# Kernel tuning notes

Hardware: AMD Instinct MI355X
Metric: run time of the kernel (lower is better)

Reference implementation:

```python
import jax, jax.numpy as jnp
import numpy as np

B, N, D_IN, D_OUT, D_EDGE = 2, 512, 128, 128, 32
NEG_SLOPE = 0.2  # GATv2 LeakyReLU default


def _glorot(k, shape):
    lim = np.sqrt(6.0 / (shape[0] + shape[1]))
    return jax.random.uniform(k, shape, jnp.float32, -lim, lim)


def setup_inputs() -> dict:
    key = jax.random.key(0)
    ks = jax.random.split(key, 8)
    return {
        "node_features": jax.random.normal(ks[0], (B, N, D_IN), jnp.float32),
        "adj": jax.random.uniform(ks[1], (B, N, N)) < 0.1,  # sparse-ish dense adjacency
        "edge_features": jax.random.normal(ks[2], (B, N, N, D_EDGE), jnp.float32),
        "mask": jnp.ones((B, N), dtype=bool),
        "W_l": _glorot(ks[3], (D_IN, D_OUT)),   # source (lin_l)
        "b_l": jnp.zeros((D_OUT,), jnp.float32),
        "W_r": _glorot(ks[4], (D_IN, D_OUT)),   # target (lin_r)
        "b_r": jnp.zeros((D_OUT,), jnp.float32),
        "W_e": _glorot(ks[5], (D_EDGE, D_OUT)), # lin_edge (no bias)
        "att": _glorot(ks[6], (1, D_OUT))[0],   # attention vector [D_OUT]
        "bias": jnp.zeros((D_OUT,), jnp.float32),
    }


def _gatv2_dense(x, adj, e, mask, W_l, b_l, W_r, b_r, W_e, att, bias):
    # add self-loops (dense GAT convention)
    adj = adj | jnp.eye(N, dtype=bool)
    x_l = x @ W_l + b_l              # [B,N,D] source transform
    x_r = x @ W_r + b_r              # [B,N,D] target transform
    e_t = e @ W_e                    # [B,N,N,D] edge transform
    # edge (j -> i): pre[b,i,j,:] = x_l[b,j] + x_r[b,i] + e_t[b,i,j]
    pre = x_l[:, None, :, :] + x_r[:, :, None, :] + e_t
    score = jnp.einsum('bijd,d->bij', jax.nn.leaky_relu(pre, NEG_SLOPE), att)
    score = jnp.where(adj, score, -jnp.inf)
    alpha = jax.nn.softmax(score, axis=-1)  # softmax over neighbors j
    out = jnp.einsum('bij,bjd->bid', alpha, x_l) + bias
    return jnp.where(mask[:, :, None], out, 0.0)


def reference(node_features, adj, edge_features, mask, W_l, b_l, W_r, b_r, W_e, att, bias):
    return jax.nn.silu(
        _gatv2_dense(node_features, adj, edge_features, mask,
                     W_l, b_l, W_r, b_r, W_e, att, bias)
    )
```

## Files before the change

kernel.cpp:

```cpp
#include <hip/hip_runtime.h>
#include <math.h>

#define BATCH 2
#define NNODE 512
#define DIN   128
#define DOUT  128
#define DE    32
#define NEG   0.2f
#define TI    8
#define TJ    64
#define TIB   8

typedef __attribute__((ext_vector_type(8))) short bf16x8;
typedef __attribute__((ext_vector_type(4))) float f32x4;

__device__ inline short f2bf(float f) {
    union { float f; unsigned u; } v; v.f = f;
    unsigned r = v.u + 0x7fffu + ((v.u >> 16) & 1u);
    return (short)(r >> 16);
}

__global__ __launch_bounds__(256) void xlr_kernel(
    const float* __restrict__ x,  const float* __restrict__ Wl,
    const float* __restrict__ bl, const float* __restrict__ Wr,
    const float* __restrict__ br, float* __restrict__ xl,
    float* __restrict__ xr)
{
    const int r0 = blockIdx.x * 4;
    const int d  = threadIdx.x & 127;
    const int hv = threadIdx.x >> 7;
    __shared__ float xs[4][DIN];
    for (int idx = threadIdx.x; idx < 4 * DIN; idx += 256)
        xs[idx >> 7][idx & 127] = x[(size_t)r0 * DIN + idx];
    __syncthreads();
    const int ra = 2 * hv, rb = ra + 1;
    float al0 = bl[d], al1 = al0, ar0 = br[d], ar1 = ar0;
    #pragma unroll 4
    for (int k = 0; k < DIN; ++k) {
        const float wl = Wl[k * DOUT + d], wr = Wr[k * DOUT + d];
        const float xa = xs[ra][k], xb = xs[rb][k];
        al0 = fmaf(xa, wl, al0); al1 = fmaf(xb, wl, al1);
        ar0 = fmaf(xa, wr, ar0); ar1 = fmaf(xb, wr, ar1);
    }
    xl[(size_t)(r0 + ra) * DOUT + d] = al0;
    xl[(size_t)(r0 + rb) * DOUT + d] = al1;
    xr[(size_t)(r0 + ra) * DOUT + d] = ar0;
    xr[(size_t)(r0 + rb) * DOUT + d] = ar1;
}

__global__ __launch_bounds__(256, 4) void score_kernel(
    const float* __restrict__ xl, const float* __restrict__ xr,
    const void* __restrict__ adjv, const float* __restrict__ e,
    const float* __restrict__ We, const float* __restrict__ att,
    float* __restrict__ sc)
{
    const int bid = blockIdx.x;
    const int jT  = bid & 7;
    const int iT  = (bid >> 3) & 63;
    const int b   = bid >> 9;
    const int i0  = iT * TI, j0 = jT * TJ;
    const int t    = threadIdx.x;
    const int wave = t >> 6;
    const int lane = t & 63;
    const int col  = lane & 15;
    const int g    = lane >> 4;

    __shared__ short WeT_s[DOUT][DE];
    __shared__ float xr_s[TI][DOUT];
    __shared__ float att_s[DOUT];
    __shared__ int   mflag[2];

    if (t < 2) mflag[t] = 0;
    for (int idx = t; idx < DE * DOUT; idx += 256) {
        const int k = idx >> 7, d = idx & 127;
        WeT_s[d][k] = f2bf(We[idx]);
    }
    for (int idx = t; idx < TI * DOUT; idx += 256) {
        const int ii = idx >> 7, d = idx & 127;
        xr_s[ii][d] = xr[(size_t)(b * NNODE + i0 + ii) * DOUT + d];
    }
    if (t < DOUT) att_s[t] = att[t];
    {
        const unsigned* aw = (const unsigned*)adjv;
        unsigned sawF = 0, sawG = 0;
        #pragma unroll
        for (int k = 0; k < 16; ++k) {
            const unsigned w = aw[t + 256 * k];
            sawF |= (w == 0x3f800000u);
            sawG |= (w > 1u);
        }
        if (sawF) atomicOr(&mflag[0], 1);
        if (sawG) atomicOr(&mflag[1], 1);
    }

    float xlv[32];
    {
        const float* xb = xl + (size_t)(b * NNODE + j0 + wave * 16 + g * 4) * DOUT + col;
        #pragma unroll
        for (int dt = 0; dt < 8; ++dt)
            #pragma unroll
            for (int r = 0; r < 4; ++r)
                xlv[dt * 4 + r] = xb[(size_t)r * DOUT + dt * 16];
    }
    __syncthreads();
    const int byteMode = (!mflag[0] && mflag[1]) ? 1 : 0;

    bf16x8 bf[8];
    float  atv[8];
    #pragma unroll
    for (int dt = 0; dt < 8; ++dt) {
        bf[dt]  = *(const bf16x8*)&WeT_s[dt * 16 + col][g * 8];
        atv[dt] = att_s[dt * 16 + col];
    }

    const int jw = j0 + wave * 16;
    const float* ebase = e + ((size_t)(b * NNODE + i0) * NNODE + jw + col) * DE + g * 8;
    const size_t estep = (size_t)NNODE * DE;

    f32x4 a0 = *(const f32x4*)ebase;
    f32x4 a1 = *(const f32x4*)(ebase + 4);

    for (int i = 0; i < TI; ++i) {
        f32x4 a0n, a1n;
        if (i + 1 < TI) {
            const float* apn = ebase + (size_t)(i + 1) * estep;
            a0n = *(const f32x4*)apn;
            a1n = *(const f32x4*)(apn + 4);
        }
        bf16x8 af;
        af[0] = f2bf(a0[0]); af[1] = f2bf(a0[1]);
        af[2] = f2bf(a0[2]); af[3] = f2bf(a0[3]);
        af[4] = f2bf(a1[0]); af[5] = f2bf(a1[1]);
        af[6] = f2bf(a1[2]); af[7] = f2bf(a1[3]);

        const f32x4 z = {0.f, 0.f, 0.f, 0.f};
        float part[4] = {0.f, 0.f, 0.f, 0.f};
        #pragma unroll
        for (int dt = 0; dt < 8; ++dt) {
            const f32x4 c = __builtin_amdgcn_mfma_f32_16x16x32_bf16(af, bf[dt], z, 0, 0, 0);
            const float xrv = xr_s[i][dt * 16 + col];
            #pragma unroll
            for (int r = 0; r < 4; ++r) {
                float p = c[r] + xrv + xlv[dt * 4 + r];
                p = fmaxf(p, NEG * p);
                part[r] = fmaf(atv[dt], p, part[r]);
            }
        }
        #pragma unroll
        for (int r = 0; r < 4; ++r) {
            part[r] += __shfl_xor(part[r], 1, 64);
            part[r] += __shfl_xor(part[r], 2, 64);
            part[r] += __shfl_xor(part[r], 4, 64);
            part[r] += __shfl_xor(part[r], 8, 64);
        }
        if (col == 0) {
            const int ig = i0 + i;
            const int jb = jw + g * 4;
            const unsigned char* aB = (const unsigned char*)adjv + (size_t)(b * NNODE + ig) * NNODE;
            const unsigned*      aW = (const unsigned*)adjv + (size_t)(b * NNODE + ig) * NNODE;
            float4 v;
            float* vp = (float*)&v;
            #pragma unroll
            for (int r = 0; r < 4; ++r) {
                const int j = jb + r;
                const bool conn = (j == ig) ||
                    (byteMode ? (aB[j] != 0) : (aW[j] != 0));
                vp[r] = conn ? part[r] : -1e30f;
            }
            *(float4*)&sc[(size_t)(b * NNODE + ig) * NNODE + jb] = v;
        }
        a0 = a0n; a1 = a1n;
    }
}

__global__ __launch_bounds__(256) void agg_kernel(
    const float* __restrict__ xl, const float* __restrict__ sc,
    const void* __restrict__ adjv, const void* __restrict__ maskv,
    const float* __restrict__ bias, float* __restrict__ out)
{
    const int bid = blockIdx.x;
    const int dh  = bid & 1;
    const int iT  = (bid >> 1) & 63;
    const int b   = bid >> 7;
    const int i0  = iT * TIB, d0 = dh * 64;
    const int t    = threadIdx.x;
    const int wave = t >> 6;
    const int lane = t & 63;

    __shared__ float al_s[TIB][NNODE];
    __shared__ int   mflag[2];

    if (t < 2) mflag[t] = 0;
    {
        const unsigned* aw = (const unsigned*)adjv;
        unsigned sawF = 0, sawG = 0;
        #pragma unroll
        for (int k = 0; k < 16; ++k) {
            const unsigned w = aw[t + 256 * k];
            sawF |= (w == 0x3f800000u);
            sawG |= (w > 1u);
        }
        if (sawF) atomicOr(&mflag[0], 1);
        if (sawG) atomicOr(&mflag[1], 1);
    }
    for (int idx = t; idx < TIB * NNODE; idx += 256) {
        const int r = idx >> 9, jj = idx & 511;
        al_s[r][jj] = sc[(size_t)(b * NNODE + i0 + r) * NNODE + jj];
    }
    __syncthreads();
    const int byteMode = (!mflag[0] && mflag[1]) ? 1 : 0;

    float invs[2];
    #pragma unroll
    for (int q = 0; q < 2; ++q) {
        const int rr = wave + 4 * q;
        float v[8], m = -1e30f;
        #pragma unroll
        for (int k = 0; k < 8; ++k) {
            v[k] = al_s[rr][lane + 64 * k];
            m = fmaxf(m, v[k]);
        }
        #pragma unroll
        for (int off = 32; off; off >>= 1) m = fmaxf(m, __shfl_xor(m, off, 64));
        float s = 0.f;
        #pragma unroll
        for (int k = 0; k < 8; ++k) {
            const float ex = __expf(v[k] - m);
            al_s[rr][lane + 64 * k] = ex;
            s += ex;
        }
        #pragma unroll
        for (int off = 32; off; off >>= 1) s += __shfl_xor(s, off, 64);
        invs[q] = 1.f / s;
    }

    const int d = d0 + lane;
    const float* xb = xl + (size_t)b * NNODE * DOUT + d;
    float a0 = 0.f, a0b = 0.f, a1 = 0.f, a1b = 0.f;
    for (int j = 0; j < NNODE; j += 2) {
        const float x0 = xb[(size_t)j * DOUT];
        const float x1 = xb[(size_t)(j + 1) * DOUT];
        a0  = fmaf(al_s[wave][j],     x0, a0);
        a0b = fmaf(al_s[wave][j + 1], x1, a0b);
        a1  = fmaf(al_s[wave + 4][j],     x0, a1);
        a1b = fmaf(al_s[wave + 4][j + 1], x1, a1b);
    }
    const float bv = bias[d];
    #pragma unroll
    for (int q = 0; q < 2; ++q) {
        const int row = i0 + wave + 4 * q;
        const int mi  = b * NNODE + row;
        const bool mv = byteMode ? (((const unsigned char*)maskv)[mi] != 0)
                                 : (((const unsigned*)maskv)[mi] != 0);
        float val = (q == 0 ? a0 + a0b : a1 + a1b) * invs[q] + bv;
        if (!mv) val = 0.f;
        val = val / (1.f + __expf(-val));
        out[(size_t)mi * DOUT + d] = val;
    }
}

extern "C" void kernel_launch(void* const* d_in, const int* in_sizes, int n_in,
                              void* d_out, int out_size, void* d_ws, size_t ws_size,
                              hipStream_t stream)
{
    const float* x    = (const float*)d_in[0];
    const void*  adj  = d_in[1];
    const float* e    = (const float*)d_in[2];
    const void*  mask = d_in[3];
    const float* Wl   = (const float*)d_in[4];
    const float* bl   = (const float*)d_in[5];
    const float* Wr   = (const float*)d_in[6];
    const float* br   = (const float*)d_in[7];
    const float* We   = (const float*)d_in[8];
    const float* att  = (const float*)d_in[9];
    const float* bias = (const float*)d_in[10];
    float*       out  = (float*)d_out;

    float* xl = (float*)d_ws;
    float* xr = xl + (size_t)BATCH * NNODE * DOUT;
    float* sc = xr + (size_t)BATCH * NNODE * DOUT;

    xlr_kernel<<<(BATCH * NNODE) / 4, 256, 0, stream>>>(x, Wl, bl, Wr, br, xl, xr);
    score_kernel<<<BATCH * (NNODE / TI) * (NNODE / TJ), 256, 0, stream>>>(
        xl, xr, adj, e, We, att, sc);
    agg_kernel<<<BATCH * (NNODE / TIB) * 2, 256, 0, stream>>>(
        xl, sc, adj, mask, bias, out);
}
```

Measured before the change: 58.58 us.

## Fold x_l into MFMA accumulator, use DPP row reductions, halve agg row tile

```diff
diff --git a/kernel.cpp b/kernel.cpp
--- a/kernel.cpp
+++ b/kernel.cpp
@@ -9,7 +9,7 @@
 #define NEG   0.2f
 #define TI    8
 #define TJ    64
-#define TIB   8
+#define TIB   4
 
 typedef __attribute__((ext_vector_type(8))) short bf16x8;
 typedef __attribute__((ext_vector_type(4))) float f32x4;
@@ -18,6 +18,19 @@
     union { float f; unsigned u; } v; v.f = f;
     unsigned r = v.u + 0x7fffu + ((v.u >> 16) & 1u);
     return (short)(r >> 16);
+}
+
+template<int CTRL>
+__device__ inline float dpp_add(float x) {
+    const int y = __builtin_amdgcn_update_dpp(0, __float_as_int(x), CTRL, 0xF, 0xF, false);
+    return x + __int_as_float(y);
+}
+__device__ inline float row16_sum(float x) {
+    x = dpp_add<0x128>(x);
+    x = dpp_add<0x124>(x);
+    x = dpp_add<0x122>(x);
+    x = dpp_add<0x121>(x);
+    return x;
 }
 
 __global__ __launch_bounds__(256) void xlr_kernel(
@@ -93,14 +106,14 @@
         if (sawG) atomicOr(&mflag[1], 1);
     }
 
-    float xlv[32];
+    f32x4 xlv4[8];
     {
         const float* xb = xl + (size_t)(b * NNODE + j0 + wave * 16 + g * 4) * DOUT + col;
         #pragma unroll
         for (int dt = 0; dt < 8; ++dt)
             #pragma unroll
             for (int r = 0; r < 4; ++r)
-                xlv[dt * 4 + r] = xb[(size_t)r * DOUT + dt * 16];
+                xlv4[dt][r] = xb[(size_t)r * DOUT + dt * 16];
     }
     __syncthreads();
     const int byteMode = (!mflag[0] && mflag[1]) ? 1 : 0;
@@ -133,26 +146,22 @@
         af[4] = f2bf(a1[0]); af[5] = f2bf(a1[1]);
         af[6] = f2bf(a1[2]); af[7] = f2bf(a1[3]);
 
-        const f32x4 z = {0.f, 0.f, 0.f, 0.f};
         float part[4] = {0.f, 0.f, 0.f, 0.f};
         #pragma unroll
         for (int dt = 0; dt < 8; ++dt) {
-            const f32x4 c = __builtin_amdgcn_mfma_f32_16x16x32_bf16(af, bf[dt], z, 0, 0, 0);
+            const f32x4 c = __builtin_amdgcn_mfma_f32_16x16x32_bf16(af, bf[dt], xlv4[dt], 0, 0, 0);
             const float xrv = xr_s[i][dt * 16 + col];
             #pragma unroll
             for (int r = 0; r < 4; ++r) {
-                float p = c[r] + xrv + xlv[dt * 4 + r];
+                float p = c[r] + xrv;
                 p = fmaxf(p, NEG * p);
                 part[r] = fmaf(atv[dt], p, part[r]);
             }
         }
         #pragma unroll
-        for (int r = 0; r < 4; ++r) {
-            part[r] += __shfl_xor(part[r], 1, 64);
-            part[r] += __shfl_xor(part[r], 2, 64);
-            part[r] += __shfl_xor(part[r], 4, 64);
-            part[r] += __shfl_xor(part[r], 8, 64);
-        }
+        for (int r = 0; r < 4; ++r)
+            part[r] = row16_sum(part[r]);
+
         if (col == 0) {
             const int ig = i0 + i;
             const int jb = jw + g * 4;
@@ -180,8 +189,8 @@
 {
     const int bid = blockIdx.x;
     const int dh  = bid & 1;
-    const int iT  = (bid >> 1) & 63;
-    const int b   = bid >> 7;
+    const int iT  = (bid >> 1) & 127;
+    const int b   = bid >> 8;
     const int i0  = iT * TIB, d0 = dh * 64;
     const int t    = threadIdx.x;
     const int wave = t >> 6;
@@ -210,14 +219,12 @@
     __syncthreads();
     const int byteMode = (!mflag[0] && mflag[1]) ? 1 : 0;
 
-    float invs[2];
-    #pragma unroll
-    for (int q = 0; q < 2; ++q) {
-        const int rr = wave + 4 * q;
+    float inv;
+    {
         float v[8], m = -1e30f;
         #pragma unroll
         for (int k = 0; k < 8; ++k) {
-            v[k] = al_s[rr][lane + 64 * k];
+            v[k] = al_s[wave][lane + 64 * k];
             m = fmaxf(m, v[k]);
         }
         #pragma unroll
@@ -226,37 +233,31 @@
         #pragma unroll
         for (int k = 0; k < 8; ++k) {
             const float ex = __expf(v[k] - m);
-            al_s[rr][lane + 64 * k] = ex;
+            al_s[wave][lane + 64 * k] = ex;
             s += ex;
         }
         #pragma unroll
         for (int off = 32; off; off >>= 1) s += __shfl_xor(s, off, 64);
-        invs[q] = 1.f / s;
+        inv = 1.f / s;
     }
 
     const int d = d0 + lane;
     const float* xb = xl + (size_t)b * NNODE * DOUT + d;
-    float a0 = 0.f, a0b = 0.f, a1 = 0.f, a1b = 0.f;
-    for (int j = 0; j < NNODE; j += 2) {
-        const float x0 = xb[(size_t)j * DOUT];
-        const float x1 = xb[(size_t)(j + 1) * DOUT];
-        a0  = fmaf(al_s[wave][j],     x0, a0);
-        a0b = fmaf(al_s[wave][j + 1], x1, a0b);
-        a1  = fmaf(al_s[wave + 4][j],     x0, a1);
-        a1b = fmaf(al_s[wave + 4][j + 1], x1, a1b);
-    }
-    const float bv = bias[d];
-    #pragma unroll
-    for (int q = 0; q < 2; ++q) {
-        const int row = i0 + wave + 4 * q;
-        const int mi  = b * NNODE + row;
-        const bool mv = byteMode ? (((const unsigned char*)maskv)[mi] != 0)
-                                 : (((const unsigned*)maskv)[mi] != 0);
-        float val = (q == 0 ? a0 + a0b : a1 + a1b) * invs[q] + bv;
-        if (!mv) val = 0.f;
-        val = val / (1.f + __expf(-val));
-        out[(size_t)mi * DOUT + d] = val;
-    }
+    float ac0 = 0.f, ac1 = 0.f, ac2 = 0.f, ac3 = 0.f;
+    #pragma unroll 2
+    for (int j = 0; j < NNODE; j += 4) {
+        ac0 = fmaf(al_s[wave][j],     xb[(size_t)j * DOUT],       ac0);
+        ac1 = fmaf(al_s[wave][j + 1], xb[(size_t)(j + 1) * DOUT], ac1);
+        ac2 = fmaf(al_s[wave][j + 2], xb[(size_t)(j + 2) * DOUT], ac2);
+        ac3 = fmaf(al_s[wave][j + 3], xb[(size_t)(j + 3) * DOUT], ac3);
+    }
+    const int mi = b * NNODE + i0 + wave;
+    const bool mv = byteMode ? (((const unsigned char*)maskv)[mi] != 0)
+                             : (((const unsigned*)maskv)[mi] != 0);
+    float val = ((ac0 + ac1) + (ac2 + ac3)) * inv + bias[d];
+    if (!mv) val = 0.f;
+    val = val / (1.f + __expf(-val));
+    out[(size_t)mi * DOUT + d] = val;
 }
 
 extern "C" void kernel_launch(void* const* d_in, const int* in_sizes, int n_in,
```

Measured after the change: 64.44 us. 1.1x slower.
